# Optimization experiments

Hardware: AMD Instinct MI355X
Metric: run time of the kernel (lower is better)

The kernel has to match this reference:

```python
import jax, jax.numpy as jnp
import numpy as np

B, D1, D2, D3, E = 32, 32, 32, 8, 256

def setup_inputs() -> dict:
    key = jax.random.key(0)
    k1, k2 = jax.random.split(key)
    c_embeds = jax.random.normal(k1, (B, D1, D2, D3, E), dtype=jnp.float32)
    s_embeds = jax.random.normal(k2, (B, E), dtype=jnp.float32)
    return {"c_embeds": c_embeds, "s_embeds": s_embeds}

def reference(c_embeds, s_embeds):
    # dot product of each grid-cell context embedding with the per-batch
    # segment embedding; fused broadcast-multiply-reduce over E.
    b = c_embeds.shape[0]
    ctx = c_embeds.reshape(b, -1, c_embeds.shape[-1])   # [B, N, E]
    out = jnp.einsum('bne,be->bn', ctx, s_embeds)       # [B, N]
    return out
```

## Files before the change

### kernel.cpp

```cpp
#include <hip/hip_runtime.h>


constexpr int kLogN = 13;
constexpr int kF4PerRow = 64;

__global__ __launch_bounds__(256) void ctx_seg_score_kernel(
    const float* __restrict__ c,
    const float* __restrict__ s,
    float* __restrict__ out,
    int total_outputs)
{
    const int tid  = blockIdx.x * blockDim.x + threadIdx.x;
    const int w    = tid >> 6;
    const int lane = tid & 63;
    if (w >= total_outputs) return;

    const int b = w >> kLogN;

    const float4* __restrict__ c4p = reinterpret_cast<const float4*>(c);
    const float4* __restrict__ s4p = reinterpret_cast<const float4*>(s);

    const float4 c4 = c4p[(size_t)w * kF4PerRow + lane];
    const float4 s4 = s4p[(size_t)b * kF4PerRow + lane];

    float v = c4.x * s4.x + c4.y * s4.y + c4.z * s4.z + c4.w * s4.w;

    #pragma unroll
    for (int off = 32; off > 0; off >>= 1)
        v += __shfl_xor(v, off, 64);

    if (lane == 0) out[w] = v;
}

extern "C" void kernel_launch(void* const* d_in, const int* in_sizes, int n_in,
                              void* d_out, int out_size, void* d_ws, size_t ws_size,
                              hipStream_t stream) {
    const float* c = (const float*)d_in[0];
    const float* s = (const float*)d_in[1];
    float* out = (float*)d_out;

    const int total_outputs = out_size;
    const int threads = 256;
    const int waves_needed = total_outputs;
    const int blocks = (waves_needed * 64 + threads - 1) / threads;

    ctx_seg_score_kernel<<<blocks, threads, 0, stream>>>(c, s, out, total_outputs);
}
```

Before: 338.5 us.

## Process 32 rows per wave with unrolled loads and batched reductions

Each wavefront now handles 32 consecutive output rows instead of one. The segment vector is loaded once per wave and reused, four rows are loaded together, and their four partial sums are reduced with interleaved shuffles before one float4 store. This cuts redundant s loads and the per-row launch overhead and adds memory-level parallelism. The cost is far fewer waves (8192 instead of 262144), which may lower occupancy for a bandwidth-bound kernel.

New measurement: 353.7 us. 4.5% more time.

```diff
diff --git a/kernel.cpp b/kernel.cpp
--- a/kernel.cpp
+++ b/kernel.cpp
@@ -1,35 +1,55 @@
 #include <hip/hip_runtime.h>
 
 
-constexpr int kLogN = 13;
-constexpr int kF4PerRow = 64;
+constexpr int kLogN       = 13;
+constexpr int kF4PerRow   = 64;
+constexpr int kRowsPerWave = 32;
+constexpr int kUnroll      = 4;
 
 __global__ __launch_bounds__(256) void ctx_seg_score_kernel(
     const float* __restrict__ c,
     const float* __restrict__ s,
     float* __restrict__ out,
-    int total_outputs)
+    int total_rows)
 {
     const int tid  = blockIdx.x * blockDim.x + threadIdx.x;
-    const int w    = tid >> 6;
+    const int wave = tid >> 6;
     const int lane = tid & 63;
-    if (w >= total_outputs) return;
 
-    const int b = w >> kLogN;
+    const int row0 = wave * kRowsPerWave;
+    if (row0 >= total_rows) return;
+
+    const int b = row0 >> kLogN;
 
     const float4* __restrict__ c4p = reinterpret_cast<const float4*>(c);
-    const float4* __restrict__ s4p = reinterpret_cast<const float4*>(s);
+    const float4  s4 = reinterpret_cast<const float4*>(s)[(size_t)b * kF4PerRow + lane];
 
-    const float4 c4 = c4p[(size_t)w * kF4PerRow + lane];
-    const float4 s4 = s4p[(size_t)b * kF4PerRow + lane];
+    #pragma unroll 2
+    for (int i = 0; i < kRowsPerWave; i += kUnroll) {
+        const int r = row0 + i;
 
-    float v = c4.x * s4.x + c4.y * s4.y + c4.z * s4.z + c4.w * s4.w;
+        float4 a[kUnroll];
+        #pragma unroll
+        for (int u = 0; u < kUnroll; ++u)
+            a[u] = c4p[(size_t)(r + u) * kF4PerRow + lane];
 
-    #pragma unroll
-    for (int off = 32; off > 0; off >>= 1)
-        v += __shfl_xor(v, off, 64);
+        float4 p;
+        p.x = fmaf(a[0].x, s4.x, fmaf(a[0].y, s4.y, fmaf(a[0].z, s4.z, a[0].w * s4.w)));
+        p.y = fmaf(a[1].x, s4.x, fmaf(a[1].y, s4.y, fmaf(a[1].z, s4.z, a[1].w * s4.w)));
+        p.z = fmaf(a[2].x, s4.x, fmaf(a[2].y, s4.y, fmaf(a[2].z, s4.z, a[2].w * s4.w)));
+        p.w = fmaf(a[3].x, s4.x, fmaf(a[3].y, s4.y, fmaf(a[3].z, s4.z, a[3].w * s4.w)));
 
-    if (lane == 0) out[w] = v;
+        #pragma unroll
+        for (int off = 32; off > 0; off >>= 1) {
+            p.x += __shfl_xor(p.x, off, 64);
+            p.y += __shfl_xor(p.y, off, 64);
+            p.z += __shfl_xor(p.z, off, 64);
+            p.w += __shfl_xor(p.w, off, 64);
+        }
+
+        if (lane == 0)
+            reinterpret_cast<float4*>(out)[r >> 2] = p;
+    }
 }
 
 extern "C" void kernel_launch(void* const* d_in, const int* in_sizes, int n_in,
@@ -39,10 +59,10 @@
     const float* s = (const float*)d_in[1];
     float* out = (float*)d_out;
 
-    const int total_outputs = out_size;
+    const int total_rows = out_size;
+    const int waves = (total_rows + kRowsPerWave - 1) / kRowsPerWave;
     const int threads = 256;
-    const int waves_needed = total_outputs;
-    const int blocks = (waves_needed * 64 + threads - 1) / threads;
+    const int blocks = (waves * 64 + threads - 1) / threads;
 
-    ctx_seg_score_kernel<<<blocks, threads, 0, stream>>>(c, s, out, total_outputs);
+    ctx_seg_score_kernel<<<blocks, threads, 0, stream>>>(c, s, out, total_rows);
 }
```

## Process eight rows per wave with grid-stride loop and butterfly merge reduction

Applied to the files above, without the earlier changes.

Each wave now handles eight consecutive rows per iteration of a persistent grid-stride loop over a fixed grid. It issues eight nontemporal float4 loads up front and reduces the eight partial sums with a transpose-style butterfly. This cuts the shuffle count per row and keeps more memory requests in flight. Launch overhead from millions of tiny waves is removed, at the cost of more registers and reliance on the row count being a multiple of eight.

New measurement: 327.6 us. 3.2% less time.

```diff
diff --git a/kernel.cpp b/kernel.cpp
--- a/kernel.cpp
+++ b/kernel.cpp
@@ -1,35 +1,71 @@
 #include <hip/hip_runtime.h>
 
 
-constexpr int kLogN = 13;
-constexpr int kF4PerRow = 64;
+typedef float f32x4 __attribute__((ext_vector_type(4)));
 
-__global__ __launch_bounds__(256) void ctx_seg_score_kernel(
+constexpr int kLogN        = 13;
+constexpr int kF4PerRow    = 64;
+constexpr int kRowsPerIter = 8;
+constexpr int kBlocks      = 1024;
+constexpr int kThreads     = 256;
+
+__device__ __forceinline__ float lane_merge(float a, float b, int sel, int off) {
+    float send = sel ? a : b;
+    float recv = __shfl_xor(send, off, 64);
+    return (sel ? b : a) + recv;
+}
+
+__global__ __launch_bounds__(kThreads) void ctx_seg_score_kernel(
     const float* __restrict__ c,
     const float* __restrict__ s,
     float* __restrict__ out,
-    int total_outputs)
+    int total_rows)
 {
-    const int tid  = blockIdx.x * blockDim.x + threadIdx.x;
-    const int w    = tid >> 6;
-    const int lane = tid & 63;
-    if (w >= total_outputs) return;
+    const int lane   = threadIdx.x & 63;
+    const int gwave  = (blockIdx.x * blockDim.x + threadIdx.x) >> 6;
+    const int nwaves = (gridDim.x * blockDim.x) >> 6;
 
-    const int b = w >> kLogN;
-
-    const float4* __restrict__ c4p = reinterpret_cast<const float4*>(c);
+    const f32x4* __restrict__ c4p = reinterpret_cast<const f32x4*>(c);
     const float4* __restrict__ s4p = reinterpret_cast<const float4*>(s);
 
-    const float4 c4 = c4p[(size_t)w * kF4PerRow + lane];
-    const float4 s4 = s4p[(size_t)b * kF4PerRow + lane];
+    const int sel1 = lane & 1;
+    const int sel2 = (lane >> 1) & 1;
+    const int sel4 = (lane >> 2) & 1;
 
-    float v = c4.x * s4.x + c4.y * s4.y + c4.z * s4.z + c4.w * s4.w;
+    for (int r0 = gwave * kRowsPerIter; r0 < total_rows;
+         r0 += nwaves * kRowsPerIter) {
 
-    #pragma unroll
-    for (int off = 32; off > 0; off >>= 1)
-        v += __shfl_xor(v, off, 64);
+        const int b = r0 >> kLogN;
+        const float4 s4 = s4p[b * kF4PerRow + lane];
 
-    if (lane == 0) out[w] = v;
+        f32x4 a[kRowsPerIter];
+        #pragma unroll
+        for (int u = 0; u < kRowsPerIter; ++u)
+            a[u] = __builtin_nontemporal_load(
+                &c4p[(size_t)(r0 + u) * kF4PerRow + lane]);
+
+        float p[kRowsPerIter];
+        #pragma unroll
+        for (int u = 0; u < kRowsPerIter; ++u)
+            p[u] = fmaf(a[u].x, s4.x,
+                   fmaf(a[u].y, s4.y,
+                   fmaf(a[u].z, s4.z, a[u].w * s4.w)));
+
+        float v01 = lane_merge(p[0], p[1], sel1, 1);
+        float v23 = lane_merge(p[2], p[3], sel1, 1);
+        float v45 = lane_merge(p[4], p[5], sel1, 1);
+        float v67 = lane_merge(p[6], p[7], sel1, 1);
+        float w03 = lane_merge(v01, v23, sel2, 2);
+        float w47 = lane_merge(v45, v67, sel2, 2);
+        float v   = lane_merge(w03, w47, sel4, 4);
+
+        v += __shfl_xor(v, 8, 64);
+        v += __shfl_xor(v, 16, 64);
+        v += __shfl_xor(v, 32, 64);
+
+        if (lane < kRowsPerIter)
+            out[r0 + lane] = v;
+    }
 }
 
 extern "C" void kernel_launch(void* const* d_in, const int* in_sizes, int n_in,
@@ -39,10 +75,5 @@
     const float* s = (const float*)d_in[1];
     float* out = (float*)d_out;
 
-    const int total_outputs = out_size;
-    const int threads = 256;
-    const int waves_needed = total_outputs;
-    const int blocks = (waves_needed * 64 + threads - 1) / threads;
-
-    ctx_seg_score_kernel<<<blocks, threads, 0, stream>>>(c, s, out, total_outputs);
+    ctx_seg_score_kernel<<<kBlocks, kThreads, 0, stream>>>(c, s, out, out_size);
 }
```
